# Kernel tuning notes

Measured on AMD Instinct MI355X. Metric: run time of the kernel, lower is better.

Reference implementation:

```python
import jax, jax.numpy as jnp
import numpy as np
import math

B, N, DIM, H, DH = 2, 2048, 768, 12, 64
NUM_BUCKETS, MAX_DIST = 32, 128


def _rel_pos_bucket(n):
    # causal bucketing as in T5RelativePositionBias._relative_position_bucket
    rel = jnp.arange(n)[None, :] - jnp.arange(n)[:, None]          # k_pos - q_pos
    neg = jnp.maximum(-rel, 0)                                     # n = max(-rel, 0)
    max_exact = NUM_BUCKETS // 2
    is_small = neg < max_exact
    val_large = max_exact + (
        jnp.log(jnp.maximum(neg, 1).astype(jnp.float32) / max_exact)
        / math.log(MAX_DIST / max_exact) * (NUM_BUCKETS - max_exact)
    ).astype(jnp.int32)
    val_large = jnp.minimum(val_large, NUM_BUCKETS - 1)
    return jnp.where(is_small, neg, val_large)                     # [n, n] int32


def setup_inputs() -> dict:
    key = jax.random.key(0)
    ks = jax.random.split(key, 6)
    s = DIM ** -0.5
    x = jax.random.normal(ks[0], (B, N, DIM), jnp.float32)
    mask = jnp.ones((B, N), dtype=bool)
    Wq = jax.random.normal(ks[1], (DIM, H * DH), jnp.float32) * s
    Wk = jax.random.normal(ks[2], (DIM, H * DH), jnp.float32) * s
    Wv = jax.random.normal(ks[3], (DIM, H * DH), jnp.float32) * s
    Wo = jax.random.normal(ks[4], (H * DH, DIM), jnp.float32) * s
    rel_emb = jax.random.normal(ks[5], (NUM_BUCKETS, H), jnp.float32) * 0.02
    return {"x": x, "mask": mask, "Wq": Wq, "Wk": Wk, "Wv": Wv, "Wo": Wo, "rel_emb": rel_emb}


def reference(x, mask, Wq, Wk, Wv, Wo, rel_emb):
    b, n, _ = x.shape
    scale = DH ** -0.5
    # projections -> [b, h, n, d]
    q = (x @ Wq).reshape(b, n, H, DH).transpose(0, 2, 1, 3) * scale
    k = (x @ Wk).reshape(b, n, H, DH).transpose(0, 2, 1, 3)
    v = (x @ Wv).reshape(b, n, H, DH).transpose(0, 2, 1, 3)
    sim = jnp.einsum('bhid,bhjd->bhij', q, k)                      # [b, h, n, n]
    # relative position bias, also scaled by dim_head**-0.5
    bias = rel_emb[_rel_pos_bucket(n)]                             # [n, n, h]
    sim = sim + jnp.transpose(bias, (2, 0, 1))[None] * scale
    mask_value = -jnp.finfo(sim.dtype).max
    # key/query padding mask: ~mask[:, None, :, None] masks rows (query dim)
    sim = jnp.where(mask[:, None, :, None], sim, mask_value)
    causal = jnp.triu(jnp.ones((n, n), dtype=bool), 1)
    sim = jnp.where(causal[None, None], mask_value, sim)
    attn = jax.nn.softmax(sim, axis=-1)
    out = jnp.einsum('bhij,bhjd->bhid', attn, v)                   # [b, h, n, d]
    out = out.transpose(0, 2, 1, 3).reshape(b, n, H * DH)
    return out @ Wo
```

## Files before the change

### kernel.cpp

```cpp
#include <hip/hip_runtime.h>
#include <math.h>

#define NSEQ 2048
#define HDIM 768
#define NHEAD 12
#define DHEAD 64
#define CHUNK 6
#define NJOBS 51
#define EXP_C1 1.44269504f
#define EXP_C0 -17.3123405f

typedef __attribute__((ext_vector_type(8))) short short8;
typedef __attribute__((ext_vector_type(4))) float f32x4;

static __device__ __forceinline__ unsigned short f2bf(float x) {
    unsigned int u = __float_as_uint(x);
    unsigned int r = (u + 0x7fffu + ((u >> 16) & 1u)) >> 16;
    return (unsigned short)r;
}
static __device__ __forceinline__ float bf2f(unsigned short u) {
    return __uint_as_float(((unsigned int)u) << 16);
}

#define GLD_LDS16(g, l)                                                  \
    __builtin_amdgcn_global_load_lds(                                    \
        (const __attribute__((address_space(1))) void*)(g),              \
        (__attribute__((address_space(3))) void*)(l), 16, 0, 0)

__global__ __launch_bounds__(256) void prep(const float* __restrict__ X,
                                            const float* __restrict__ Wq,
                                            const float* __restrict__ Wk,
                                            const float* __restrict__ Wv,
                                            const float* __restrict__ Wo,
                                            const float* __restrict__ relemb,
                                            unsigned short* __restrict__ Xb,
                                            unsigned short* __restrict__ Wt,
                                            unsigned short* __restrict__ rbg) {
    __shared__ float tb[64][65];
    const int z = blockIdx.x;
    if (z < 576) {
        const int wsel = z / 144, tt = z % 144;
        const int n0 = (tt % 12) * 64, k0 = (tt / 12) * 64;
        const float* W = (wsel == 0) ? Wq : (wsel == 1) ? Wk : (wsel == 2) ? Wv : Wo;
        const float scale = (wsel == 0) ? 0.125f : 1.0f;
        unsigned short* dst = Wt + (size_t)wsel * HDIM * HDIM;
        const int r = threadIdx.x >> 4;
        const int c4 = (threadIdx.x & 15) * 4;
#pragma unroll
        for (int i = 0; i < 4; i++) {
            int row = i * 16 + r;
            float4 v = *(const float4*)(W + (size_t)(k0 + row) * HDIM + n0 + c4);
            tb[c4 + 0][row] = v.x * scale;
            tb[c4 + 1][row] = v.y * scale;
            tb[c4 + 2][row] = v.z * scale;
            tb[c4 + 3][row] = v.w * scale;
        }
        __syncthreads();
#pragma unroll
        for (int i = 0; i < 4; i++) {
            int row = i * 16 + r;
            ushort4 o;
            o.x = f2bf(tb[row][c4 + 0]);
            o.y = f2bf(tb[row][c4 + 1]);
            o.z = f2bf(tb[row][c4 + 2]);
            o.w = f2bf(tb[row][c4 + 3]);
            *(ushort4*)(dst + (size_t)(n0 + row) * HDIM + k0 + c4) = o;
        }
    } else if (z < 960) {
        int base = (z - 576) * 2048 + threadIdx.x;
#pragma unroll
        for (int u = 0; u < 8; u++) {
            int f = base + u * 256;
            float4 v = ((const float4*)X)[f];
            ushort4 o;
            o.x = f2bf(v.x); o.y = f2bf(v.y); o.z = f2bf(v.z); o.w = f2bf(v.w);
            ((ushort4*)Xb)[f] = o;
        }
    } else {
        int idx = (z - 960) * 256 + threadIdx.x;
        int h = idx >> 11;
        int d = idx & (NSEQ - 1);
        int bucket;
        if (d < 16) {
            bucket = d;
        } else {
            float v = logf((float)d * (1.0f / 16.0f)) * (16.0f / logf(8.0f));
            bucket = 16 + (int)v;
            if (bucket > 31) bucket = 31;
        }
        rbg[h * NSEQ + d] = f2bf(relemb[bucket * NHEAD + h] * 0.125f);
    }
}

template <int MODE, int MT>
__global__ __launch_bounds__(256) void gemm_bt(const unsigned short* __restrict__ A,
                                               const unsigned short* __restrict__ Bt,
                                               void* __restrict__ Cout) {
    __shared__ unsigned short As[(MT * 32) * 32];
    __shared__ unsigned short Bs[128 * 32];

    const int tid = threadIdx.x;
    const int w = tid >> 6, lane = tid & 63;
    const int ln = lane & 15, qd = lane >> 4;
    const int wm = w >> 1, wn = w & 1;
    const int mat = blockIdx.x / (HDIM / 128);
    const int n0 = (blockIdx.x % (HDIM / 128)) * 128;
    const int m0 = blockIdx.y * (MT * 32);
    const unsigned short* Bm = Bt + (size_t)mat * HDIM * HDIM;

    const int scol = (lane & 3) * 8;
    const int arow = w * (MT * 8) + (lane >> 2);
    const int brow = w * 32 + (lane >> 2);
    const unsigned short* agp = A + (size_t)(m0 + arow) * HDIM + scol;
    const unsigned short* bgp = Bm + (size_t)(n0 + brow) * HDIM + scol;
    unsigned short* al = As + (w * (MT * 8)) * 32;
    unsigned short* bl = Bs + (w * 32) * 32;

    f32x4 acc[MT][4];
#pragma unroll
    for (int i = 0; i < MT; i++)
#pragma unroll
        for (int j = 0; j < 4; j++) acc[i][j] = (f32x4){0.f, 0.f, 0.f, 0.f};

    for (int k0 = 0; k0 < HDIM; k0 += 32) {
        __syncthreads();
        GLD_LDS16(agp + k0, al);
        if (MT == 4) GLD_LDS16(agp + 16 * HDIM + k0, al + 16 * 32);
        GLD_LDS16(bgp + k0, bl);
        GLD_LDS16(bgp + 16 * HDIM + k0, bl + 16 * 32);
        __syncthreads();

        short8 af[MT], bf[4];
#pragma unroll
        for (int mt = 0; mt < MT; mt++)
            af[mt] = *(const short8*)&As[(wm * (MT * 16) + mt * 16 + ln) * 32 + qd * 8];
#pragma unroll
        for (int nt = 0; nt < 4; nt++)
            bf[nt] = *(const short8*)&Bs[(wn * 64 + nt * 16 + ln) * 32 + qd * 8];
#pragma unroll
        for (int mt = 0; mt < MT; mt++)
#pragma unroll
            for (int nt = 0; nt < 4; nt++)
                acc[mt][nt] = __builtin_amdgcn_mfma_f32_16x16x32_bf16(
                    af[mt], bf[nt], acc[mt][nt], 0, 0, 0);
    }

    if constexpr (MODE == 0) {
        float* C = (float*)Cout;
#pragma unroll
        for (int mt = 0; mt < MT; mt++)
#pragma unroll
            for (int r = 0; r < 4; r++) {
                int m = m0 + wm * (MT * 16) + mt * 16 + qd * 4 + r;
#pragma unroll
                for (int nt = 0; nt < 4; nt++) {
                    int n = n0 + wn * 64 + nt * 16 + ln;
                    C[(size_t)m * HDIM + n] = acc[mt][nt][r];
                }
            }
    } else {
        const size_t QKVE = (size_t)2 * NHEAD * NSEQ * DHEAD;
        if (mat < 2) {
            unsigned short* dstm = (unsigned short*)Cout + (size_t)mat * QKVE;
#pragma unroll
            for (int mt = 0; mt < MT; mt++)
#pragma unroll
                for (int r = 0; r < 4; r++) {
                    int m = m0 + wm * (MT * 16) + mt * 16 + qd * 4 + r;
                    int b = m >> 11, tok = m & (NSEQ - 1);
#pragma unroll
                    for (int nt = 0; nt < 4; nt++) {
                        int col = n0 + wn * 64 + nt * 16 + ln;
                        int h = col >> 6, dh = col & 63;
                        dstm[((size_t)(b * NHEAD + h) * NSEQ + tok) * DHEAD + dh] =
                            f2bf(acc[mt][nt][r]);
                    }
                }
        } else {
            __shared__ unsigned short Ts[128 * 72];
#pragma unroll
            for (int mt = 0; mt < MT; mt++)
#pragma unroll
                for (int nt = 0; nt < 4; nt++) {
                    int col = wn * 64 + nt * 16 + ln;
#pragma unroll
                    for (int r = 0; r < 4; r++) {
                        int row = wm * (MT * 16) + mt * 16 + qd * 4 + r;
                        Ts[col * 72 + row] = f2bf(acc[mt][nt][r]);
                    }
                }
            __syncthreads();
            unsigned short* dstm = (unsigned short*)Cout + 2 * QKVE;
            const int b = m0 >> 11, tokb = m0 & (NSEQ - 1);
#pragma unroll
            for (int i = 0; i < 4; i++) {
                int idx = i * 256 + tid;
                int col = idx >> 3;
                int t8 = idx & 7;
                short8 vv = *(const short8*)&Ts[col * 72 + t8 * 8];
                int gcol = n0 + col;
                int h = gcol >> 6, dh = gcol & 63;
                *(short8*)(dstm + ((size_t)(b * NHEAD + h) * DHEAD + dh) * NSEQ +
                           tokb + t8 * 8) = vv;
            }
        }
    }
}

__global__ __launch_bounds__(256) void attn_mfma(const unsigned short* __restrict__ Q,
                                                 const unsigned short* __restrict__ K,
                                                 const unsigned short* __restrict__ Vt_g,
                                                 const unsigned short* __restrict__ rbg,
                                                 unsigned short* __restrict__ AO,
                                                 unsigned short* __restrict__ Of,
                                                 float* __restrict__ Pl) {
    __shared__ __align__(16) unsigned short Ks[64 * 72];
    __shared__ __align__(16) unsigned short Vt[64 * 72];
    __shared__ __align__(16) unsigned short Ps[4 * 32 * 72];
    __shared__ __align__(16) unsigned short rbs[512];

    const int tid = threadIdx.x;
    const int w = tid >> 6;
    const int lane = tid & 63;
    const int ln = lane & 15;
    const int qd = lane >> 4;
    const int job = NJOBS - 1 - blockIdx.x;
    const int h = blockIdx.y;
    const int b = blockIdx.z;

    int qt = 0, cb = 0;
    for (;;) {
        int c = (2 * qt + 2 + CHUNK - 1) / CHUNK;
        if (job < cb + c) break;
        cb += c;
        qt++;
    }
    const int c = (2 * qt + 2 + CHUNK - 1) / CHUNK;
    const int jd = job - cb;
    const int ntk = 2 * qt + 2;
    const int t0 = ntk * jd / c, t1 = ntk * (jd + 1) / c;
    const int i0 = qt * 128;

    const int bhl = b * NHEAD + h;
    const size_t bh = (size_t)bhl;
    const unsigned short* Kb = K + bh * NSEQ * DHEAD;
    const unsigned short* Vg = Vt_g + bh * DHEAD * NSEQ;

    const int wbase = i0 - t1 * 64 + 1;
    const unsigned short NEG = f2bf(-1e30f);
#pragma unroll
    for (int u = 0; u < 2; u++) {
        int idx = u * 256 + tid;
        int d = wbase + idx;
        int dc = d < 0 ? 0 : (d > NSEQ - 1 ? NSEQ - 1 : d);
        rbs[idx] = (d < 0) ? NEG : rbg[h * NSEQ + dc];
    }

    short8 qf[2][2];
#pragma unroll
    for (int rg = 0; rg < 2; rg++) {
        const unsigned short* qrow =
            Q + (bh * NSEQ + i0 + w * 32 + rg * 16 + ln) * DHEAD;
        qf[rg][0] = *(const short8*)(qrow + qd * 8);
        qf[rg][1] = *(const short8*)(qrow + 32 + qd * 8);
    }

    short8 ones;
#pragma unroll
    for (int e = 0; e < 8; e++) ones[e] = (short)0x3F80;

    f32x4 o[2][4];
#pragma unroll
    for (int rg = 0; rg < 2; rg++)
#pragma unroll
        for (int cc = 0; cc < 4; cc++) o[rg][cc] = (f32x4){0.f, 0.f, 0.f, 0.f};
    f32x4 o4[2] = {{0.f, 0.f, 0.f, 0.f}, {0.f, 0.f, 0.f, 0.f}};

    int bqw[2];
#pragma unroll
    for (int rg = 0; rg < 2; rg++)
        bqw[rg] = i0 + w * 32 + rg * 16 + qd * 4 - ln - wbase;

    unsigned short* Pw = Ps + w * 32 * 72;

    const int sr = tid >> 3;
    const int sc = (tid & 7) * 8;
    short8 kp[2], vp[2];
    {
        const int jb = t0 * 64;
#pragma unroll
        for (int u = 0; u < 2; u++) {
            kp[u] = *(const short8*)(Kb + (size_t)(jb + u * 32 + sr) * DHEAD + sc);
            vp[u] = *(const short8*)(Vg + (size_t)(u * 32 + sr) * NSEQ + jb + sc);
        }
    }

    for (int t = t0; t < t1; t++) {
        const int jt = t * 64;
        __syncthreads();
#pragma unroll
        for (int u = 0; u < 2; u++) {
            *(short8*)&Ks[(u * 32 + sr) * 72 + sc] = kp[u];
            *(short8*)&Vt[(u * 32 + sr) * 72 + sc] = vp[u];
        }
        __syncthreads();
        if (t + 1 < t1) {
            const int jn = jt + 64;
#pragma unroll
            for (int u = 0; u < 2; u++) {
                kp[u] = *(const short8*)(Kb + (size_t)(jn + u * 32 + sr) * DHEAD + sc);
                vp[u] = *(const short8*)(Vg + (size_t)(u * 32 + sr) * NSEQ + jn + sc);
            }
        }

        short8 kf[4][2];
#pragma unroll
        for (int cc = 0; cc < 4; cc++) {
            kf[cc][0] = *(const short8*)&Ks[(cc * 16 + ln) * 72 + qd * 8];
            kf[cc][1] = *(const short8*)&Ks[(cc * 16 + ln) * 72 + 32 + qd * 8];
        }

#pragma unroll
        for (int rg = 0; rg < 2; rg++) {
            f32x4 s[4] = {{0.f, 0.f, 0.f, 0.f}, {0.f, 0.f, 0.f, 0.f},
                          {0.f, 0.f, 0.f, 0.f}, {0.f, 0.f, 0.f, 0.f}};
#pragma unroll
            for (int cc = 0; cc < 4; cc++) {
                s[cc] = __builtin_amdgcn_mfma_f32_16x16x32_bf16(qf[rg][0], kf[cc][0],
                                                               s[cc], 0, 0, 0);
                s[cc] = __builtin_amdgcn_mfma_f32_16x16x32_bf16(qf[rg][1], kf[cc][1],
                                                               s[cc], 0, 0, 0);
            }
#pragma unroll
            for (int cc = 0; cc < 4; cc++) {
                const int ib = bqw[rg] - jt - cc * 16;
#pragma unroll
                for (int r = 0; r < 4; r++) {
                    float sv = s[cc][r] + bf2f(rbs[ib + r]);
                    float p = __builtin_amdgcn_exp2f(__fmaf_rn(sv, EXP_C1, EXP_C0));
                    Pw[(rg * 16 + qd * 4 + r) * 72 + cc * 16 + ln] = f2bf(p);
                }
            }
        }

        short8 vf[4][2];
#pragma unroll
        for (int cc = 0; cc < 4; cc++) {
            vf[cc][0] = *(const short8*)&Vt[(cc * 16 + ln) * 72 + qd * 8];
            vf[cc][1] = *(const short8*)&Vt[(cc * 16 + ln) * 72 + 32 + qd * 8];
        }

#pragma unroll
        for (int rg = 0; rg < 2; rg++) {
            short8 pa0 = *(const short8*)(Pw + (rg * 16 + ln) * 72 + qd * 8);
            short8 pa1 = *(const short8*)(Pw + (rg * 16 + ln) * 72 + 32 + qd * 8);
#pragma unroll
            for (int cc = 0; cc < 4; cc++) {
                o[rg][cc] = __builtin_amdgcn_mfma_f32_16x16x32_bf16(pa0, vf[cc][0],
                                                                    o[rg][cc], 0, 0, 0);
                o[rg][cc] = __builtin_amdgcn_mfma_f32_16x16x32_bf16(pa1, vf[cc][1],
                                                                    o[rg][cc], 0, 0, 0);
            }
            o4[rg] = __builtin_amdgcn_mfma_f32_16x16x32_bf16(pa0, ones, o4[rg], 0, 0, 0);
            o4[rg] = __builtin_amdgcn_mfma_f32_16x16x32_bf16(pa1, ones, o4[rg], 0, 0, 0);
        }
    }

    if (job < 3) {
#pragma unroll
        for (int rg = 0; rg < 2; rg++) {
            unsigned short* aop = AO +
                ((size_t)(b * NSEQ) + i0 + w * 32 + rg * 16 + qd * 4) * HDIM +
                h * DHEAD + ln;
#pragma unroll
            for (int r = 0; r < 4; r++) {
                float inv = 1.0f / o4[rg][r];
#pragma unroll
                for (int cc = 0; cc < 4; cc++)
                    aop[(size_t)r * HDIM + cc * 16] = f2bf(o[rg][cc][r] * inv);
            }
        }
    } else {
        const size_t gc = (size_t)bhl * NJOBS + job;
#pragma unroll
        for (int rg = 0; rg < 2; rg++) {
            const int rowl = w * 32 + rg * 16 + qd * 4;
            unsigned short* po = Of + (gc * 128 + rowl) * 64 + ln;
#pragma unroll
            for (int r = 0; r < 4; r++) {
                float inv = 1.0f / o4[rg][r];
#pragma unroll
                for (int cc = 0; cc < 4; cc++)
                    po[(size_t)r * 64 + cc * 16] = f2bf(o[rg][cc][r] * inv);
            }
            if (ln == 0) {
#pragma unroll
                for (int r = 0; r < 4; r++) Pl[gc * 128 + rowl + r] = o4[rg][r];
            }
        }
    }
}

__global__ __launch_bounds__(256) void attn_merge(const unsigned short* __restrict__ Of,
                                                  const float* __restrict__ Pl,
                                                  unsigned short* __restrict__ AO) {
    const int tid = threadIdx.x;
    const int row_g = blockIdx.x * 4 + (tid >> 6);
    const int dh = tid & 63;
    const int bhl = row_g / (NSEQ - 384);
    const int tok = 384 + row_g % (NSEQ - 384);
    const int b = bhl / NHEAD, h = bhl % NHEAD;
    const int g2 = tok >> 7;

    int cb = 0;
    for (int qq = 0; qq < g2; qq++) cb += (2 * qq + 2 + CHUNK - 1) / CHUNK;
    const int c = (2 * g2 + 2 + CHUNK - 1) / CHUNK;
    const int rowl = tok & 127;

    float acc = 0.f, W = 0.f;
    for (int i = 0; i < c; i++) {
        size_t gc = (size_t)bhl * NJOBS + cb + i;
        float l = Pl[gc * 128 + rowl];
        acc += l * bf2f(Of[(gc * 128 + rowl) * 64 + dh]);
        W += l;
    }
    AO[((size_t)(b * NSEQ) + tok) * HDIM + h * DHEAD + dh] = f2bf(acc / W);
}

extern "C" void kernel_launch(void* const* d_in, const int* in_sizes, int n_in,
                              void* d_out, int out_size, void* d_ws, size_t ws_size,
                              hipStream_t stream) {
    const float* x      = (const float*)d_in[0];
    const float* Wq     = (const float*)d_in[2];
    const float* Wk     = (const float*)d_in[3];
    const float* Wv     = (const float*)d_in[4];
    const float* Wo     = (const float*)d_in[5];
    const float* relemb = (const float*)d_in[6];
    float* out = (float*)d_out;

    const size_t QKV = (size_t)2 * NHEAD * NSEQ * DHEAD;
    const size_t NCHUNK = (size_t)24 * NJOBS;
    unsigned short* q   = (unsigned short*)d_ws;
    unsigned short* k   = q + QKV;
    unsigned short* vT  = k + QKV;
    unsigned short* aob = vT + QKV;
    unsigned short* xb  = aob + QKV;
    unsigned short* wt  = xb + QKV;
    unsigned short* rbg = wt + (size_t)4 * HDIM * HDIM;
    unsigned short* Of  = rbg + (size_t)NHEAD * NSEQ;
    float* Pl = (float*)(Of + NCHUNK * 128 * 64);

    prep<<<1056, 256, 0, stream>>>(x, Wq, Wk, Wv, Wo, relemb, xb, wt, rbg);

    gemm_bt<1, 2><<<dim3(3 * HDIM / 128, (2 * NSEQ) / 64), 256, 0, stream>>>(
        xb, wt, q);

    attn_mfma<<<dim3(NJOBS, NHEAD, 2), 256, 0, stream>>>(q, k, vT, rbg, aob, Of, Pl);

    attn_merge<<<(24 * (NSEQ - 384)) / 4, 256, 0, stream>>>(Of, Pl, aob);

    gemm_bt<0, 2><<<dim3(HDIM / 128, (2 * NSEQ) / 64), 256, 0, stream>>>(
        aob, wt + (size_t)3 * HDIM * HDIM, out);
}
```

Measured before the change: 185.3 us.

## Load K/V MFMA fragments directly from global memory, dropping LDS staging

Removes the shared-memory K and V tiles, the register prefetch double-buffer and the two per-iteration barriers. Each wave now reads its K and V MFMA fragments straight from global memory, relying on L1/L2 caching because all four waves read the same tile. The job order is also flipped so blocks are dispatched in ascending job index instead of heaviest-first. This trades barrier and LDS traffic for redundant global loads with no prefetch, so global-load latency is exposed, and the reversed order may hurt load balance.

```diff
diff --git a/kernel.cpp b/kernel.cpp
--- a/kernel.cpp
+++ b/kernel.cpp
@@ -214,8 +214,6 @@
                                                  unsigned short* __restrict__ AO,
                                                  unsigned short* __restrict__ Of,
                                                  float* __restrict__ Pl) {
-    __shared__ __align__(16) unsigned short Ks[64 * 72];
-    __shared__ __align__(16) unsigned short Vt[64 * 72];
     __shared__ __align__(16) unsigned short Ps[4 * 32 * 72];
     __shared__ __align__(16) unsigned short rbs[512];
 
@@ -224,7 +222,7 @@
     const int lane = tid & 63;
     const int ln = lane & 15;
     const int qd = lane >> 4;
-    const int job = NJOBS - 1 - blockIdx.x;
+    const int job = blockIdx.x;
     const int h = blockIdx.y;
     const int b = blockIdx.z;
 
@@ -283,41 +281,17 @@
 
     unsigned short* Pw = Ps + w * 32 * 72;
 
-    const int sr = tid >> 3;
-    const int sc = (tid & 7) * 8;
-    short8 kp[2], vp[2];
-    {
-        const int jb = t0 * 64;
-#pragma unroll
-        for (int u = 0; u < 2; u++) {
-            kp[u] = *(const short8*)(Kb + (size_t)(jb + u * 32 + sr) * DHEAD + sc);
-            vp[u] = *(const short8*)(Vg + (size_t)(u * 32 + sr) * NSEQ + jb + sc);
-        }
-    }
+    __syncthreads();
 
     for (int t = t0; t < t1; t++) {
         const int jt = t * 64;
-        __syncthreads();
-#pragma unroll
-        for (int u = 0; u < 2; u++) {
-            *(short8*)&Ks[(u * 32 + sr) * 72 + sc] = kp[u];
-            *(short8*)&Vt[(u * 32 + sr) * 72 + sc] = vp[u];
-        }
-        __syncthreads();
-        if (t + 1 < t1) {
-            const int jn = jt + 64;
-#pragma unroll
-            for (int u = 0; u < 2; u++) {
-                kp[u] = *(const short8*)(Kb + (size_t)(jn + u * 32 + sr) * DHEAD + sc);
-                vp[u] = *(const short8*)(Vg + (size_t)(u * 32 + sr) * NSEQ + jn + sc);
-            }
-        }
 
         short8 kf[4][2];
 #pragma unroll
         for (int cc = 0; cc < 4; cc++) {
-            kf[cc][0] = *(const short8*)&Ks[(cc * 16 + ln) * 72 + qd * 8];
-            kf[cc][1] = *(const short8*)&Ks[(cc * 16 + ln) * 72 + 32 + qd * 8];
+            const unsigned short* kr = Kb + (size_t)(jt + cc * 16 + ln) * DHEAD;
+            kf[cc][0] = *(const short8*)(kr + qd * 8);
+            kf[cc][1] = *(const short8*)(kr + 32 + qd * 8);
         }
 
 #pragma unroll
@@ -346,8 +320,9 @@
         short8 vf[4][2];
 #pragma unroll
         for (int cc = 0; cc < 4; cc++) {
-            vf[cc][0] = *(const short8*)&Vt[(cc * 16 + ln) * 72 + qd * 8];
-            vf[cc][1] = *(const short8*)&Vt[(cc * 16 + ln) * 72 + 32 + qd * 8];
+            const unsigned short* vr = Vg + (size_t)(cc * 16 + ln) * NSEQ + jt;
+            vf[cc][0] = *(const short8*)(vr + qd * 8);
+            vf[cc][1] = *(const short8*)(vr + 32 + qd * 8);
         }
 
 #pragma unroll
```

New measurement: 213.1 us. 1.15x slower.
